# Kernel tuning notes

Measured on AMD Instinct MI355X. Metric: run time of the kernel, lower is better.

The kernel has to match this reference:

```python
import jax, jax.numpy as jnp
import numpy as np

BS = 4
N_NODES = 10000
N_FEAT = 64
HID = 128
N_LAYERS = 4
HID_FC = 512
N_CLASSES = 10
N_EDGES = 160000


def setup_inputs() -> dict:
    key = jax.random.key(0)
    ks = jax.random.split(key, 10)
    x = jax.random.normal(ks[0], (BS, N_NODES, N_FEAT), jnp.float32)
    edge_index = jax.random.randint(ks[1], (2, N_EDGES), 0, N_NODES, dtype=jnp.int32)
    # batch[b*N_NODES + i] = b, matching x.view(num_nodes*bs, -1) row-major flatten
    batch = jnp.repeat(jnp.arange(BS, dtype=jnp.int32), N_NODES)
    W1 = jax.random.normal(ks[2], (N_FEAT, HID), jnp.float32) * (N_FEAT ** -0.5)
    b1 = jax.random.normal(ks[3], (HID,), jnp.float32) * 0.01
    Ws = jax.random.normal(ks[4], (N_LAYERS - 1, HID, HID), jnp.float32) * (HID ** -0.5)
    bconvs = jax.random.normal(ks[5], (N_LAYERS - 1, HID), jnp.float32) * 0.01
    lin1_w = jax.random.normal(ks[6], (N_LAYERS * HID, HID_FC), jnp.float32) * ((N_LAYERS * HID) ** -0.5)
    lin1_b = jax.random.normal(ks[7], (HID_FC,), jnp.float32) * 0.01
    lin2_w = jax.random.normal(ks[8], (HID_FC, N_CLASSES), jnp.float32) * (HID_FC ** -0.5)
    lin2_b = jax.random.normal(ks[9], (N_CLASSES,), jnp.float32) * 0.01
    return {"x": x, "edge_index": edge_index, "batch": batch,
            "W1": W1, "b1": b1, "Ws": Ws, "bconvs": bconvs,
            "lin1_w": lin1_w, "lin1_b": lin1_b, "lin2_w": lin2_w, "lin2_b": lin2_b}


def _gcn_norm(edge_index, n):
    # PyG GCNConv: add self-loops, symmetric normalization D^-1/2 (A+I) D^-1/2
    loops = jnp.arange(n, dtype=edge_index.dtype)
    src = jnp.concatenate([edge_index[0], loops])
    dst = jnp.concatenate([edge_index[1], loops])
    deg = jnp.zeros((n,), jnp.float32).at[dst].add(1.0)
    dinv = jnp.where(deg > 0, jax.lax.rsqrt(deg), 0.0)
    return src, dst, dinv[src] * dinv[dst]


def reference(x, edge_index, batch, W1, b1, Ws, bconvs, lin1_w, lin1_b, lin2_w, lin2_b):
    bs, n, _ = x.shape
    src, dst, norm = _gcn_norm(edge_index, n)

    def gcn(h, W, b):
        m = (h @ W)[:, src, :] * norm[None, :, None]          # [bs, E+n, H]
        agg = jax.vmap(lambda mm: jax.ops.segment_sum(mm, dst, num_segments=n))(m)
        return agg + b

    h = jax.nn.relu(gcn(x, W1, b1))
    xs = [h]
    for i in range(Ws.shape[0]):
        h = jax.nn.relu(gcn(h, Ws[i], bconvs[i]))
        xs.append(h)
    # torch.stack(xs, -1).view(bs, n, -1): per-channel layer interleave
    h = jnp.stack(xs, -1).reshape(bs, n, -1)                   # [bs, n, L*H]
    flat = h.reshape(bs * n, -1)
    summed = jax.ops.segment_sum(flat, batch, num_segments=bs)
    counts = jax.ops.segment_sum(jnp.ones((bs * n,), flat.dtype), batch, num_segments=bs)
    pooled = summed / counts[:, None]                          # global_mean_pool
    h = jax.nn.relu(pooled @ lin1_w + lin1_b)
    # dropout p=0.5 is inference-disabled (training=False)
    logits = h @ lin2_w + lin2_b
    return jax.nn.log_softmax(logits, axis=-1)
```

## Files before the change

### kernel.cpp

```cpp
#include <hip/hip_runtime.h>
#include <hip/hip_bf16.h>
#include <math.h>

#define N_NODES 10000
#define N_EDGES 160000
#define BS      4
#define N_TOT   (BS * N_NODES)
#define HID     128
#define NPC     10
#define CHUNKS  (N_NODES/NPC)
#define HID_FC  512
#define N_CLASSES 10
#define N_LAYERS  4
#define DEG_CAP 64

using bf16x8 = __attribute__((ext_vector_type(8))) short;
using f32x4  = __attribute__((ext_vector_type(4))) float;

__device__ __forceinline__ float bf_lo(unsigned u) { return __uint_as_float(u << 16); }
__device__ __forceinline__ float bf_hi(unsigned u) { return __uint_as_float(u & 0xffff0000u); }
__device__ __forceinline__ unsigned bf_rne(float x) {
    unsigned b = __float_as_uint(x);
    return (b + 0x7fffu + ((b >> 16) & 1u)) >> 16;
}
__device__ __forceinline__ float bf2f(unsigned hi16) { return __uint_as_float(hi16 << 16); }


__global__ void k_init(int4* p, int n4) {
    int i = blockIdx.x * 256 + threadIdx.x;
    if (i < n4) p[i] = make_int4(0, 0, 0, 0);
}

__global__ void k_count(const int* __restrict__ ei, int* __restrict__ counts) {
    int e = blockIdx.x * 256 + threadIdx.x;
    if (e < N_EDGES) atomicAdd(&counts[ei[N_EDGES + e]], 1);
}

__global__ void k_dinv(const int* __restrict__ counts, float* __restrict__ dinv) {
    int i = blockIdx.x * 256 + threadIdx.x;
    if (i < N_NODES) dinv[i] = rsqrtf((float)(counts[i] + 1));
}

__global__ void k_fill(const int* __restrict__ ei, int* __restrict__ cursor,
                       const float* __restrict__ dinv, int2* __restrict__ csr) {
    int e = blockIdx.x * 256 + threadIdx.x;
    if (e < N_EDGES) {
        int s = ei[e], d = ei[N_EDGES + e];
        int pos = atomicAdd(&cursor[d], 1);
        if (pos < DEG_CAP)
            csr[(d << 6) + pos] = make_int2(s, __float_as_int(dinv[s]));
    }
}

#define XB 2500
__global__ void k_cvt(const float* __restrict__ x, const float* __restrict__ W1,
                      const float* __restrict__ Ws, ushort* __restrict__ x_bf,
                      ushort* __restrict__ wt_hi, ushort* __restrict__ wt_lo) {
    int bid = blockIdx.x, t = threadIdx.x;
    if (bid < XB) {
        int i = bid * 256 + t;
        float4 v = ((const float4*)x)[i];
        ushort4 o;
        o.x = (ushort)bf_rne(v.x); o.y = (ushort)bf_rne(v.y);
        o.z = (ushort)bf_rne(v.z); o.w = (ushort)bf_rne(v.w);
        ((ushort4*)x_bf)[i] = o;
    } else {
        int idx = (bid - XB) * 256 + t;
        float v;
        if (idx < 128 * 64) {
            int c = idx >> 6, k = idx & 63;
            v = W1[k * HID + c];
        } else {
            int tt = idx - 128 * 64;
            int li = tt >> 14, rem = tt & 16383;
            int c = rem >> 7, k = rem & 127;
            v = Ws[li * 16384 + k * HID + c];
        }
        unsigned hi = bf_rne(v);
        unsigned lo = bf_rne(v - bf2f(hi));
        wt_hi[idx] = (ushort)hi;
        wt_lo[idx] = (ushort)lo;
    }
}

template<int K>
__global__ __launch_bounds__(256) void k_mm(const ushort* __restrict__ A,
                                            const ushort* __restrict__ Bt_hi,
                                            const ushort* __restrict__ Bt_lo,
                                            ushort* __restrict__ outB) {
    constexpr int NS = K / 32;
    const int lane = threadIdx.x & 63;
    const int w    = threadIdx.x >> 6;
    const int row_base = blockIdx.x * 128 + w * 32;
    const int lr = lane & 15, lg = lane >> 4;

    bf16x8 a[2][NS];
    #pragma unroll
    for (int rh = 0; rh < 2; ++rh) {
        int r = row_base + rh * 16 + lr;
        if (r > N_TOT - 1) r = N_TOT - 1;
        const ushort* ap = A + (size_t)r * K + lg * 8;
        #pragma unroll
        for (int s = 0; s < NS; ++s)
            a[rh][s] = *(const bf16x8*)(ap + s * 32);
    }

    f32x4 acc[2][8];
    #pragma unroll
    for (int rh = 0; rh < 2; ++rh)
        #pragma unroll
        for (int n = 0; n < 8; ++n)
            acc[rh][n] = (f32x4){0.f, 0.f, 0.f, 0.f};

    #pragma unroll
    for (int n = 0; n < 8; ++n) {
        const ushort* bp = Bt_hi + (size_t)(n * 16 + lr) * K + lg * 8;
        const ushort* bq = Bt_lo + (size_t)(n * 16 + lr) * K + lg * 8;
        #pragma unroll
        for (int s = 0; s < NS; ++s) {
            bf16x8 bh = *(const bf16x8*)(bp + s * 32);
            bf16x8 bl = *(const bf16x8*)(bq + s * 32);
            acc[0][n] = __builtin_amdgcn_mfma_f32_16x16x32_bf16(a[0][s], bh, acc[0][n], 0, 0, 0);
            acc[1][n] = __builtin_amdgcn_mfma_f32_16x16x32_bf16(a[1][s], bh, acc[1][n], 0, 0, 0);
            acc[0][n] = __builtin_amdgcn_mfma_f32_16x16x32_bf16(a[0][s], bl, acc[0][n], 0, 0, 0);
            acc[1][n] = __builtin_amdgcn_mfma_f32_16x16x32_bf16(a[1][s], bl, acc[1][n], 0, 0, 0);
        }
    }

    #pragma unroll
    for (int rh = 0; rh < 2; ++rh) {
        int rb = row_base + rh * 16 + lg * 4;
        #pragma unroll
        for (int n = 0; n < 8; ++n) {
            int col = n * 16 + lr;
            #pragma unroll
            for (int j = 0; j < 4; ++j) {
                int r = rb + j;
                if (r < N_TOT)
                    outB[(size_t)r * HID + col] = (ushort)bf_rne(acc[rh][n][j]);
            }
        }
    }
}

__global__ __launch_bounds__(128) void k_aggregate(const unsigned* __restrict__ tmpw,
                                                   const int* __restrict__ counts,
                                                   const int2* __restrict__ csr,
                                                   const float* __restrict__ dinv,
                                                   const float* __restrict__ bias,
                                                   unsigned* __restrict__ houtw,
                                                   float* __restrict__ partial) {
    const int id = blockIdx.x;
    const int b = (id & 7) >> 1;
    const int chunk = ((id >> 3) << 1) | (id & 1);
    const int w = threadIdx.x >> 6, l = threadIdx.x & 63;
    const unsigned* tb = tmpw + (size_t)b * N_NODES * 64;
    const float2 bv = ((const float2*)bias)[l];
    float2 pool = {0.f, 0.f};
    const int n0 = chunk * NPC + w * (NPC / 2);
    for (int n = n0; n < n0 + NPC / 2; ++n) {
        int cnt = counts[n];
        if (cnt > DEG_CAP) cnt = DEG_CAP;
        const int no = (cnt + 7) >> 3;
        const float dn = dinv[n];
        unsigned us = tb[(size_t)n * 64 + l];
        float ax[8], ay[8];
        ax[0] = dn * bf_lo(us); ay[0] = dn * bf_hi(us);
        #pragma unroll
        for (int i = 1; i < 8; ++i) { ax[i] = 0.f; ay[i] = 0.f; }
        const int4* cp = (const int4*)(csr + ((size_t)n << 6));
        for (int q = 0; q < no; ++q) {
            int4 q0 = cp[4 * q], q1 = cp[4 * q + 1], q2 = cp[4 * q + 2], q3 = cp[4 * q + 3];
            unsigned u0 = tb[(size_t)q0.x * 64 + l];
            unsigned u1 = tb[(size_t)q0.z * 64 + l];
            unsigned u2 = tb[(size_t)q1.x * 64 + l];
            unsigned u3 = tb[(size_t)q1.z * 64 + l];
            unsigned u4 = tb[(size_t)q2.x * 64 + l];
            unsigned u5 = tb[(size_t)q2.z * 64 + l];
            unsigned u6 = tb[(size_t)q3.x * 64 + l];
            unsigned u7 = tb[(size_t)q3.z * 64 + l];
            float w0 = __int_as_float(q0.y), w1 = __int_as_float(q0.w);
            float w2 = __int_as_float(q1.y), w3 = __int_as_float(q1.w);
            float w4 = __int_as_float(q2.y), w5 = __int_as_float(q2.w);
            float w6 = __int_as_float(q3.y), w7 = __int_as_float(q3.w);
            ax[0] = fmaf(w0, bf_lo(u0), ax[0]); ay[0] = fmaf(w0, bf_hi(u0), ay[0]);
            ax[1] = fmaf(w1, bf_lo(u1), ax[1]); ay[1] = fmaf(w1, bf_hi(u1), ay[1]);
            ax[2] = fmaf(w2, bf_lo(u2), ax[2]); ay[2] = fmaf(w2, bf_hi(u2), ay[2]);
            ax[3] = fmaf(w3, bf_lo(u3), ax[3]); ay[3] = fmaf(w3, bf_hi(u3), ay[3]);
            ax[4] = fmaf(w4, bf_lo(u4), ax[4]); ay[4] = fmaf(w4, bf_hi(u4), ay[4]);
            ax[5] = fmaf(w5, bf_lo(u5), ax[5]); ay[5] = fmaf(w5, bf_hi(u5), ay[5]);
            ax[6] = fmaf(w6, bf_lo(u6), ax[6]); ay[6] = fmaf(w6, bf_hi(u6), ay[6]);
            ax[7] = fmaf(w7, bf_lo(u7), ax[7]); ay[7] = fmaf(w7, bf_hi(u7), ay[7]);
        }
        float sx = ((ax[0] + ax[1]) + (ax[2] + ax[3])) + ((ax[4] + ax[5]) + (ax[6] + ax[7]));
        float sy = ((ay[0] + ay[1]) + (ay[2] + ay[3])) + ((ay[4] + ay[5]) + (ay[6] + ay[7]));
        float rx = fmaxf(fmaf(dn, sx, bv.x), 0.f);
        float ry = fmaxf(fmaf(dn, sy, bv.y), 0.f);
        houtw[((size_t)b * N_NODES + n) * 64 + l] = bf_rne(rx) | (bf_rne(ry) << 16);
        pool.x += rx; pool.y += ry;
    }
    __shared__ float2 pw[64];
    if (w == 1) pw[l] = pool;
    __syncthreads();
    if (w == 0) {
        pool.x += pw[l].x; pool.y += pw[l].y;
        ((float2*)partial)[((size_t)b * CHUNKS + chunk) * 64 + l] = pool;
    }
}

__global__ void k_reduce(const float* __restrict__ partial, float* __restrict__ pooled) {
    int l = blockIdx.x >> 2, b = blockIdx.x & 3, c = threadIdx.x;
    const float* p = partial + (size_t)(l * BS + b) * CHUNKS * HID + c;
    float s0 = 0, s1 = 0, s2 = 0, s3 = 0;
    for (int ch = 0; ch < CHUNKS; ch += 4) {
        s0 += p[(ch + 0) * HID];
        s1 += p[(ch + 1) * HID];
        s2 += p[(ch + 2) * HID];
        s3 += p[(ch + 3) * HID];
    }
    pooled[(size_t)(l * BS + b) * HID + c] = ((s0 + s1) + (s2 + s3)) * (1.0f / N_NODES);
}

__global__ __launch_bounds__(256) void k_lin1(const float* __restrict__ pooled,
                                              const float* __restrict__ w,
                                              const float* __restrict__ bias,
                                              float* __restrict__ h1) {
    __shared__ float pf[BS][HID_FC];
    __shared__ float red[8][32][BS];
    const int t = threadIdx.x;
    const int o0 = blockIdx.x * 32;
    for (int i = t; i < BS * HID_FC; i += 256) {
        int b = i >> 9, f = i & 511;
        int l = f & 3, cc = f >> 2;
        pf[b][f] = pooled[(size_t)(l * BS + b) * HID + cc];
    }
    __syncthreads();
    const int o = t & 31, kq = t >> 5;
    float acc[BS] = {0.f, 0.f, 0.f, 0.f};
    #pragma unroll 4
    for (int k = kq * 64; k < kq * 64 + 64; ++k) {
        float wv = w[(size_t)k * HID_FC + o0 + o];
        #pragma unroll
        for (int b = 0; b < BS; ++b) acc[b] = fmaf(pf[b][k], wv, acc[b]);
    }
    #pragma unroll
    for (int b = 0; b < BS; ++b) red[kq][o][b] = acc[b];
    __syncthreads();
    if (t < 128) {
        int oo = t & 31, b = t >> 5;
        float s = 0.f;
        #pragma unroll
        for (int q = 0; q < 8; ++q) s += red[q][oo][b];
        s += bias[o0 + oo];
        h1[(size_t)b * HID_FC + o0 + oo] = fmaxf(s, 0.f);
    }
}

__global__ __launch_bounds__(512) void k_lin2(const float* __restrict__ h1,
                                              const float* __restrict__ w,
                                              const float* __restrict__ bias,
                                              float* __restrict__ out) {
    const int k = threadIdx.x;
    const int lane = k & 63, wv_id = k >> 6;
    float wrow[N_CLASSES];
    #pragma unroll
    for (int c = 0; c < N_CLASSES; ++c) wrow[c] = w[k * N_CLASSES + c];
    float hv[BS];
    #pragma unroll
    for (int b = 0; b < BS; ++b) hv[b] = h1[b * HID_FC + k];
    float acc[BS][N_CLASSES];
    #pragma unroll
    for (int b = 0; b < BS; ++b)
        #pragma unroll
        for (int c = 0; c < N_CLASSES; ++c) acc[b][c] = hv[b] * wrow[c];
    #pragma unroll
    for (int off = 32; off >= 1; off >>= 1) {
        #pragma unroll
        for (int b = 0; b < BS; ++b)
            #pragma unroll
            for (int c = 0; c < N_CLASSES; ++c)
                acc[b][c] += __shfl_down(acc[b][c], off);
    }
    __shared__ float red[8][BS * N_CLASSES];
    if (lane == 0) {
        #pragma unroll
        for (int b = 0; b < BS; ++b)
            #pragma unroll
            for (int c = 0; c < N_CLASSES; ++c)
                red[wv_id][b * N_CLASSES + c] = acc[b][c];
    }
    __syncthreads();
    __shared__ float logits[BS][N_CLASSES];
    if (k < BS * N_CLASSES) {
        int b = k / N_CLASSES, c = k % N_CLASSES;
        float s = bias[c];
        #pragma unroll
        for (int q = 0; q < 8; ++q) s += red[q][k];
        logits[b][c] = s;
    }
    __syncthreads();
    if (k < BS) {
        float m = logits[k][0];
        for (int i = 1; i < N_CLASSES; ++i) m = fmaxf(m, logits[k][i]);
        float s = 0.f;
        for (int i = 0; i < N_CLASSES; ++i) s += expf(logits[k][i] - m);
        float lse = m + logf(s);
        for (int i = 0; i < N_CLASSES; ++i) out[k * N_CLASSES + i] = logits[k][i] - lse;
    }
}

extern "C" void kernel_launch(void* const* d_in, const int* in_sizes, int n_in,
                              void* d_out, int out_size, void* d_ws, size_t ws_size,
                              hipStream_t stream) {
    const float* x       = (const float*)d_in[0];
    const int*   ei      = (const int*)d_in[1];
    const float* W1      = (const float*)d_in[3];
    const float* b1      = (const float*)d_in[4];
    const float* Ws      = (const float*)d_in[5];
    const float* bconvs  = (const float*)d_in[6];
    const float* lin1_w  = (const float*)d_in[7];
    const float* lin1_b  = (const float*)d_in[8];
    const float* lin2_w  = (const float*)d_in[9];
    const float* lin2_b  = (const float*)d_in[10];
    float* out = (float*)d_out;

    char* base = (char*)d_ws;
    ushort* tmp16  = (ushort*)base;                      base += (size_t)N_TOT * HID * 2;
    ushort* hA16   = (ushort*)base;                      base += (size_t)N_TOT * HID * 2;
    ushort* x_bf   = (ushort*)base;                      base += (size_t)N_TOT * 64 * 2;
    ushort* wt_hi  = (ushort*)base;                      base += 57344 * 2;
    ushort* wt_lo  = (ushort*)base;                      base += 57344 * 2;
    float*  partial= (float*)base;                       base += (size_t)N_LAYERS * BS * CHUNKS * HID * 4;
    float*  pooled = (float*)base;                       base += N_LAYERS * BS * HID * 4;
    float*  h1     = (float*)base;                       base += BS * HID_FC * 4;
    float*  dinv   = (float*)base;                       base += N_NODES * 4;
    int*    counts = (int*)base;                         base += N_NODES * 4;
    int*    cursor = (int*)base;                         base += N_NODES * 4;
    int2*   csr    = (int2*)base;

    const int GE = (N_EDGES + 255) / 256;
    const int zero_ints = 2 * N_NODES + 2 * N_NODES * DEG_CAP;
    const int n4 = zero_ints / 4;

    k_init<<<(n4 + 255) / 256, 256, 0, stream>>>((int4*)counts, n4);
    k_count<<<GE, 256, 0, stream>>>(ei, counts);
    k_dinv<<<(N_NODES + 255) / 256, 256, 0, stream>>>(counts, dinv);
    k_fill<<<GE, 256, 0, stream>>>(ei, cursor, dinv, csr);
    k_cvt<<<XB + 224, 256, 0, stream>>>(x, W1, Ws, x_bf, wt_hi, wt_lo);

    const int agg_grid = BS * CHUNKS;
    const int mm_grid = (N_TOT + 127) / 128;

    k_mm<64><<<mm_grid, 256, 0, stream>>>(x_bf, wt_hi, wt_lo, tmp16);
    k_aggregate<<<agg_grid, 128, 0, stream>>>((unsigned*)tmp16, counts, csr, dinv, b1,
                                              (unsigned*)hA16, partial);
    for (int l = 1; l < N_LAYERS; ++l) {
        const ushort* whi = wt_hi + 8192 + (size_t)(l - 1) * 16384;
        const ushort* wlo = wt_lo + 8192 + (size_t)(l - 1) * 16384;
        const float* bl = bconvs + (size_t)(l - 1) * HID;
        k_mm<128><<<mm_grid, 256, 0, stream>>>(hA16, whi, wlo, tmp16);
        k_aggregate<<<agg_grid, 128, 0, stream>>>((unsigned*)tmp16, counts, csr, dinv, bl,
                                                  (unsigned*)hA16,
                                                  partial + (size_t)l * BS * CHUNKS * HID);
    }

    k_reduce<<<N_LAYERS * BS, HID, 0, stream>>>(partial, pooled);
    k_lin1<<<HID_FC / 32, 256, 0, stream>>>(pooled, lin1_w, lin1_b, h1);
    k_lin2<<<1, 512, 0, stream>>>(h1, lin2_w, lin2_b, out);
}
```

Measured before the change: 270.3 us.

## Replace fixed-cap CSR with compact padded CSR and interleave two-node aggregation

Builds a compact CSR with per-node rows padded to multiples of 4, allocated by an atomic bump counter, instead of a fixed 64-slot-per-node array. This removes the large zero-init and the degree cap. It fuses the zero-init, x conversion and weight split into one grid-stride prep kernel, drops the separate dinv kernel by computing rsqrt inline, and processes two nodes per iteration in the aggregation for more memory-level parallelism. NPC changes to 8. Rows are allocated by atomics, so their order is nondeterministic and locality between adjacent nodes' edge lists is lost. Padding slots rely on being zeroed (zero weight, source index 0).

```diff
diff --git a/kernel.cpp b/kernel.cpp
--- a/kernel.cpp
+++ b/kernel.cpp
@@ -7,12 +7,13 @@
 #define BS      4
 #define N_TOT   (BS * N_NODES)
 #define HID     128
-#define NPC     10
+#define NPC     8
 #define CHUNKS  (N_NODES/NPC)
 #define HID_FC  512
 #define N_CLASSES 10
 #define N_LAYERS  4
-#define DEG_CAP 64
+#define CSR_CAP 190000
+#define ZERO_INT4 102501
 
 using bf16x8 = __attribute__((ext_vector_type(8))) short;
 using f32x4  = __attribute__((ext_vector_type(4))) float;
@@ -25,61 +26,60 @@
 }
 __device__ __forceinline__ float bf2f(unsigned hi16) { return __uint_as_float(hi16 << 16); }
 
-
-__global__ void k_init(int4* p, int n4) {
-    int i = blockIdx.x * 256 + threadIdx.x;
-    if (i < n4) p[i] = make_int4(0, 0, 0, 0);
-}
-
-__global__ void k_count(const int* __restrict__ ei, int* __restrict__ counts) {
-    int e = blockIdx.x * 256 + threadIdx.x;
-    if (e < N_EDGES) atomicAdd(&counts[ei[N_EDGES + e]], 1);
-}
-
-__global__ void k_dinv(const int* __restrict__ counts, float* __restrict__ dinv) {
-    int i = blockIdx.x * 256 + threadIdx.x;
-    if (i < N_NODES) dinv[i] = rsqrtf((float)(counts[i] + 1));
-}
-
-__global__ void k_fill(const int* __restrict__ ei, int* __restrict__ cursor,
-                       const float* __restrict__ dinv, int2* __restrict__ csr) {
-    int e = blockIdx.x * 256 + threadIdx.x;
-    if (e < N_EDGES) {
-        int s = ei[e], d = ei[N_EDGES + e];
-        int pos = atomicAdd(&cursor[d], 1);
-        if (pos < DEG_CAP)
-            csr[(d << 6) + pos] = make_int2(s, __float_as_int(dinv[s]));
-    }
-}
-
-#define XB 2500
-__global__ void k_cvt(const float* __restrict__ x, const float* __restrict__ W1,
-                      const float* __restrict__ Ws, ushort* __restrict__ x_bf,
-                      ushort* __restrict__ wt_hi, ushort* __restrict__ wt_lo) {
-    int bid = blockIdx.x, t = threadIdx.x;
-    if (bid < XB) {
-        int i = bid * 256 + t;
+__global__ __launch_bounds__(256) void k_prep(const float* __restrict__ x,
+                                              const float* __restrict__ W1,
+                                              const float* __restrict__ Ws,
+                                              int4* __restrict__ zbase,
+                                              ushort* __restrict__ x_bf,
+                                              ushort* __restrict__ wt_hi,
+                                              ushort* __restrict__ wt_lo) {
+    const int gt = blockIdx.x * 256 + threadIdx.x, NT = gridDim.x * 256;
+    for (int i = gt; i < ZERO_INT4; i += NT) zbase[i] = make_int4(0, 0, 0, 0);
+    for (int i = gt; i < 640000; i += NT) {
         float4 v = ((const float4*)x)[i];
         ushort4 o;
         o.x = (ushort)bf_rne(v.x); o.y = (ushort)bf_rne(v.y);
         o.z = (ushort)bf_rne(v.z); o.w = (ushort)bf_rne(v.w);
         ((ushort4*)x_bf)[i] = o;
-    } else {
-        int idx = (bid - XB) * 256 + t;
+    }
+    for (int i = gt; i < 57344; i += NT) {
         float v;
-        if (idx < 128 * 64) {
-            int c = idx >> 6, k = idx & 63;
-            v = W1[k * HID + c];
-        } else {
-            int tt = idx - 128 * 64;
-            int li = tt >> 14, rem = tt & 16383;
+        if (i < 8192) { int c = i >> 6, k = i & 63; v = W1[k * HID + c]; }
+        else {
+            int tt = i - 8192, li = tt >> 14, rem = tt & 16383;
             int c = rem >> 7, k = rem & 127;
             v = Ws[li * 16384 + k * HID + c];
         }
         unsigned hi = bf_rne(v);
         unsigned lo = bf_rne(v - bf2f(hi));
-        wt_hi[idx] = (ushort)hi;
-        wt_lo[idx] = (ushort)lo;
+        wt_hi[i] = (ushort)hi;
+        wt_lo[i] = (ushort)lo;
+    }
+}
+
+__global__ void k_count(const int* __restrict__ ei, int* __restrict__ counts) {
+    int e = blockIdx.x * 256 + threadIdx.x;
+    if (e < N_EDGES) atomicAdd(&counts[ei[N_EDGES + e]], 1);
+}
+
+__global__ void k_alloc(const int* __restrict__ counts, int* __restrict__ row_start,
+                        int* __restrict__ g_total) {
+    int i = blockIdx.x * 256 + threadIdx.x;
+    if (i < N_NODES) {
+        int padded = (counts[i] + 3) & ~3;
+        row_start[i] = atomicAdd(g_total, padded);
+    }
+}
+
+__global__ void k_fill(const int* __restrict__ ei, const int* __restrict__ counts,
+                       const int* __restrict__ row_start, int* __restrict__ cursor,
+                       int2* __restrict__ csr) {
+    int e = blockIdx.x * 256 + threadIdx.x;
+    if (e < N_EDGES) {
+        int s = ei[e], d = ei[N_EDGES + e];
+        float ws = rsqrtf((float)(counts[s] + 1));
+        int pos = atomicAdd(&cursor[d], 1);
+        csr[row_start[d] + pos] = make_int2(s, __float_as_int(ws));
     }
 }
 
@@ -143,13 +143,13 @@
     }
 }
 
-__global__ __launch_bounds__(128) void k_aggregate(const unsigned* __restrict__ tmpw,
-                                                   const int* __restrict__ counts,
-                                                   const int2* __restrict__ csr,
-                                                   const float* __restrict__ dinv,
-                                                   const float* __restrict__ bias,
-                                                   unsigned* __restrict__ houtw,
-                                                   float* __restrict__ partial) {
+__global__ __launch_bounds__(128) void k_agg(const unsigned* __restrict__ tmpw,
+                                             const int* __restrict__ counts,
+                                             const int* __restrict__ row_start,
+                                             const int2* __restrict__ csr,
+                                             const float* __restrict__ bias,
+                                             unsigned* __restrict__ houtw,
+                                             float* __restrict__ partial) {
     const int id = blockIdx.x;
     const int b = (id & 7) >> 1;
     const int chunk = ((id >> 3) << 1) | (id & 1);
@@ -157,48 +157,74 @@
     const unsigned* tb = tmpw + (size_t)b * N_NODES * 64;
     const float2 bv = ((const float2*)bias)[l];
     float2 pool = {0.f, 0.f};
-    const int n0 = chunk * NPC + w * (NPC / 2);
-    for (int n = n0; n < n0 + NPC / 2; ++n) {
-        int cnt = counts[n];
-        if (cnt > DEG_CAP) cnt = DEG_CAP;
-        const int no = (cnt + 7) >> 3;
-        const float dn = dinv[n];
-        unsigned us = tb[(size_t)n * 64 + l];
-        float ax[8], ay[8];
-        ax[0] = dn * bf_lo(us); ay[0] = dn * bf_hi(us);
-        #pragma unroll
-        for (int i = 1; i < 8; ++i) { ax[i] = 0.f; ay[i] = 0.f; }
-        const int4* cp = (const int4*)(csr + ((size_t)n << 6));
-        for (int q = 0; q < no; ++q) {
-            int4 q0 = cp[4 * q], q1 = cp[4 * q + 1], q2 = cp[4 * q + 2], q3 = cp[4 * q + 3];
-            unsigned u0 = tb[(size_t)q0.x * 64 + l];
-            unsigned u1 = tb[(size_t)q0.z * 64 + l];
-            unsigned u2 = tb[(size_t)q1.x * 64 + l];
-            unsigned u3 = tb[(size_t)q1.z * 64 + l];
-            unsigned u4 = tb[(size_t)q2.x * 64 + l];
-            unsigned u5 = tb[(size_t)q2.z * 64 + l];
-            unsigned u6 = tb[(size_t)q3.x * 64 + l];
-            unsigned u7 = tb[(size_t)q3.z * 64 + l];
-            float w0 = __int_as_float(q0.y), w1 = __int_as_float(q0.w);
-            float w2 = __int_as_float(q1.y), w3 = __int_as_float(q1.w);
-            float w4 = __int_as_float(q2.y), w5 = __int_as_float(q2.w);
-            float w6 = __int_as_float(q3.y), w7 = __int_as_float(q3.w);
-            ax[0] = fmaf(w0, bf_lo(u0), ax[0]); ay[0] = fmaf(w0, bf_hi(u0), ay[0]);
-            ax[1] = fmaf(w1, bf_lo(u1), ax[1]); ay[1] = fmaf(w1, bf_hi(u1), ay[1]);
-            ax[2] = fmaf(w2, bf_lo(u2), ax[2]); ay[2] = fmaf(w2, bf_hi(u2), ay[2]);
-            ax[3] = fmaf(w3, bf_lo(u3), ax[3]); ay[3] = fmaf(w3, bf_hi(u3), ay[3]);
-            ax[4] = fmaf(w4, bf_lo(u4), ax[4]); ay[4] = fmaf(w4, bf_hi(u4), ay[4]);
-            ax[5] = fmaf(w5, bf_lo(u5), ax[5]); ay[5] = fmaf(w5, bf_hi(u5), ay[5]);
-            ax[6] = fmaf(w6, bf_lo(u6), ax[6]); ay[6] = fmaf(w6, bf_hi(u6), ay[6]);
-            ax[7] = fmaf(w7, bf_lo(u7), ax[7]); ay[7] = fmaf(w7, bf_hi(u7), ay[7]);
-        }
-        float sx = ((ax[0] + ax[1]) + (ax[2] + ax[3])) + ((ax[4] + ax[5]) + (ax[6] + ax[7]));
-        float sy = ((ay[0] + ay[1]) + (ay[2] + ay[3])) + ((ay[4] + ay[5]) + (ay[6] + ay[7]));
-        float rx = fmaxf(fmaf(dn, sx, bv.x), 0.f);
-        float ry = fmaxf(fmaf(dn, sy, bv.y), 0.f);
-        houtw[((size_t)b * N_NODES + n) * 64 + l] = bf_rne(rx) | (bf_rne(ry) << 16);
-        pool.x += rx; pool.y += ry;
-    }
+    const int n0 = chunk * NPC + w * 4;
+
+    #pragma unroll
+    for (int pn = 0; pn < 2; ++pn) {
+        const int nA = n0 + 2 * pn, nB = nA + 1;
+        const int cntA = counts[nA], cntB = counts[nB];
+        const int baseA = row_start[nA], baseB = row_start[nB];
+        const float dnA = rsqrtf((float)(cntA + 1));
+        const float dnB = rsqrtf((float)(cntB + 1));
+        const unsigned usA = tb[(size_t)nA * 64 + l];
+        const unsigned usB = tb[(size_t)nB * 64 + l];
+        float axA[4], ayA[4], axB[4], ayB[4];
+        axA[0] = dnA * bf_lo(usA); ayA[0] = dnA * bf_hi(usA);
+        axB[0] = dnB * bf_lo(usB); ayB[0] = dnB * bf_hi(usB);
+        #pragma unroll
+        for (int i = 1; i < 4; ++i) { axA[i] = 0.f; ayA[i] = 0.f; axB[i] = 0.f; ayB[i] = 0.f; }
+        const int nqA = (cntA + 3) >> 2, nqB = (cntB + 3) >> 2;
+        const int nq = nqA > nqB ? nqA : nqB;
+        const int4* cpA = (const int4*)(csr + baseA);
+        const int4* cpB = (const int4*)(csr + baseB);
+        for (int q = 0; q < nq; ++q) {
+            const bool doA = q < nqA, doB = q < nqB;
+            int4 qa0, qa1, qb0, qb1;
+            if (doA) { qa0 = cpA[2 * q]; qa1 = cpA[2 * q + 1]; }
+            if (doB) { qb0 = cpB[2 * q]; qb1 = cpB[2 * q + 1]; }
+            if (doA) {
+                unsigned u0 = tb[(size_t)qa0.x * 64 + l];
+                unsigned u1 = tb[(size_t)qa0.z * 64 + l];
+                unsigned u2 = tb[(size_t)qa1.x * 64 + l];
+                unsigned u3 = tb[(size_t)qa1.z * 64 + l];
+                float w0 = __int_as_float(qa0.y), w1 = __int_as_float(qa0.w);
+                float w2 = __int_as_float(qa1.y), w3 = __int_as_float(qa1.w);
+                axA[0] = fmaf(w0, bf_lo(u0), axA[0]); ayA[0] = fmaf(w0, bf_hi(u0), ayA[0]);
+                axA[1] = fmaf(w1, bf_lo(u1), axA[1]); ayA[1] = fmaf(w1, bf_hi(u1), ayA[1]);
+                axA[2] = fmaf(w2, bf_lo(u2), axA[2]); ayA[2] = fmaf(w2, bf_hi(u2), ayA[2]);
+                axA[3] = fmaf(w3, bf_lo(u3), axA[3]); ayA[3] = fmaf(w3, bf_hi(u3), ayA[3]);
+            }
+            if (doB) {
+                unsigned u0 = tb[(size_t)qb0.x * 64 + l];
+                unsigned u1 = tb[(size_t)qb0.z * 64 + l];
+                unsigned u2 = tb[(size_t)qb1.x * 64 + l];
+                unsigned u3 = tb[(size_t)qb1.z * 64 + l];
+                float w0 = __int_as_float(qb0.y), w1 = __int_as_float(qb0.w);
+                float w2 = __int_as_float(qb1.y), w3 = __int_as_float(qb1.w);
+                axB[0] = fmaf(w0, bf_lo(u0), axB[0]); ayB[0] = fmaf(w0, bf_hi(u0), ayB[0]);
+                axB[1] = fmaf(w1, bf_lo(u1), axB[1]); ayB[1] = fmaf(w1, bf_hi(u1), ayB[1]);
+                axB[2] = fmaf(w2, bf_lo(u2), axB[2]); ayB[2] = fmaf(w2, bf_hi(u2), ayB[2]);
+                axB[3] = fmaf(w3, bf_lo(u3), axB[3]); ayB[3] = fmaf(w3, bf_hi(u3), ayB[3]);
+            }
+        }
+        {
+            float sx = (axA[0] + axA[1]) + (axA[2] + axA[3]);
+            float sy = (ayA[0] + ayA[1]) + (ayA[2] + ayA[3]);
+            float rx = fmaxf(fmaf(dnA, sx, bv.x), 0.f);
+            float ry = fmaxf(fmaf(dnA, sy, bv.y), 0.f);
+            houtw[((size_t)b * N_NODES + nA) * 64 + l] = bf_rne(rx) | (bf_rne(ry) << 16);
+            pool.x += rx; pool.y += ry;
+        }
+        {
+            float sx = (axB[0] + axB[1]) + (axB[2] + axB[3]);
+            float sy = (ayB[0] + ayB[1]) + (ayB[2] + ayB[3]);
+            float rx = fmaxf(fmaf(dnB, sx, bv.x), 0.f);
+            float ry = fmaxf(fmaf(dnB, sy, bv.y), 0.f);
+            houtw[((size_t)b * N_NODES + nB) * 64 + l] = bf_rne(rx) | (bf_rne(ry) << 16);
+            pool.x += rx; pool.y += ry;
+        }
+    }
+
     __shared__ float2 pw[64];
     if (w == 1) pw[l] = pool;
     __syncthreads();
@@ -211,14 +237,12 @@
 __global__ void k_reduce(const float* __restrict__ partial, float* __restrict__ pooled) {
     int l = blockIdx.x >> 2, b = blockIdx.x & 3, c = threadIdx.x;
     const float* p = partial + (size_t)(l * BS + b) * CHUNKS * HID + c;
-    float s0 = 0, s1 = 0, s2 = 0, s3 = 0;
-    for (int ch = 0; ch < CHUNKS; ch += 4) {
+    float s0 = 0, s1 = 0;
+    for (int ch = 0; ch < CHUNKS; ch += 2) {
         s0 += p[(ch + 0) * HID];
         s1 += p[(ch + 1) * HID];
-        s2 += p[(ch + 2) * HID];
-        s3 += p[(ch + 3) * HID];
-    }
-    pooled[(size_t)(l * BS + b) * HID + c] = ((s0 + s1) + (s2 + s3)) * (1.0f / N_NODES);
+    }
+    pooled[(size_t)(l * BS + b) * HID + c] = (s0 + s1) * (1.0f / N_NODES);
 }
 
 __global__ __launch_bounds__(256) void k_lin1(const float* __restrict__ pooled,
@@ -325,43 +349,41 @@
     float* out = (float*)d_out;
 
     char* base = (char*)d_ws;
-    ushort* tmp16  = (ushort*)base;                      base += (size_t)N_TOT * HID * 2;
-    ushort* hA16   = (ushort*)base;                      base += (size_t)N_TOT * HID * 2;
-    ushort* x_bf   = (ushort*)base;                      base += (size_t)N_TOT * 64 * 2;
-    ushort* wt_hi  = (ushort*)base;                      base += 57344 * 2;
-    ushort* wt_lo  = (ushort*)base;                      base += 57344 * 2;
-    float*  partial= (float*)base;                       base += (size_t)N_LAYERS * BS * CHUNKS * HID * 4;
-    float*  pooled = (float*)base;                       base += N_LAYERS * BS * HID * 4;
-    float*  h1     = (float*)base;                       base += BS * HID_FC * 4;
-    float*  dinv   = (float*)base;                       base += N_NODES * 4;
-    int*    counts = (int*)base;                         base += N_NODES * 4;
-    int*    cursor = (int*)base;                         base += N_NODES * 4;
-    int2*   csr    = (int2*)base;
+    ushort* tmp16   = (ushort*)base;   base += (size_t)N_TOT * HID * 2;
+    ushort* hA16    = (ushort*)base;   base += (size_t)N_TOT * HID * 2;
+    ushort* x_bf    = (ushort*)base;   base += (size_t)N_TOT * 64 * 2;
+    ushort* wt_hi   = (ushort*)base;   base += 57344 * 2;
+    ushort* wt_lo   = (ushort*)base;   base += 57344 * 2;
+    float*  partial = (float*)base;    base += (size_t)N_LAYERS * BS * CHUNKS * HID * 4;
+    float*  pooled  = (float*)base;    base += N_LAYERS * BS * HID * 4;
+    float*  h1      = (float*)base;    base += BS * HID_FC * 4;
+    int*    counts    = (int*)base;    base += N_NODES * 4;
+    int*    cursor    = (int*)base;    base += N_NODES * 4;
+    int*    row_start = (int*)base;    base += N_NODES * 4;
+    int*    g_total   = (int*)base;    base += 4 * 4;
+    int2*   csr       = (int2*)base;
 
     const int GE = (N_EDGES + 255) / 256;
-    const int zero_ints = 2 * N_NODES + 2 * N_NODES * DEG_CAP;
-    const int n4 = zero_ints / 4;
-
-    k_init<<<(n4 + 255) / 256, 256, 0, stream>>>((int4*)counts, n4);
+
+    k_prep<<<1024, 256, 0, stream>>>(x, W1, Ws, (int4*)counts, x_bf, wt_hi, wt_lo);
     k_count<<<GE, 256, 0, stream>>>(ei, counts);
-    k_dinv<<<(N_NODES + 255) / 256, 256, 0, stream>>>(counts, dinv);
-    k_fill<<<GE, 256, 0, stream>>>(ei, cursor, dinv, csr);
-    k_cvt<<<XB + 224, 256, 0, stream>>>(x, W1, Ws, x_bf, wt_hi, wt_lo);
+    k_alloc<<<(N_NODES + 255) / 256, 256, 0, stream>>>(counts, row_start, g_total);
+    k_fill<<<GE, 256, 0, stream>>>(ei, counts, row_start, cursor, csr);
 
     const int agg_grid = BS * CHUNKS;
     const int mm_grid = (N_TOT + 127) / 128;
 
     k_mm<64><<<mm_grid, 256, 0, stream>>>(x_bf, wt_hi, wt_lo, tmp16);
-    k_aggregate<<<agg_grid, 128, 0, stream>>>((unsigned*)tmp16, counts, csr, dinv, b1,
-                                              (unsigned*)hA16, partial);
+    k_agg<<<agg_grid, 128, 0, stream>>>((unsigned*)tmp16, counts, row_start, csr, b1,
+                                        (unsigned*)hA16, partial);
     for (int l = 1; l < N_LAYERS; ++l) {
         const ushort* whi = wt_hi + 8192 + (size_t)(l - 1) * 16384;
         const ushort* wlo = wt_lo + 8192 + (size_t)(l - 1) * 16384;
         const float* bl = bconvs + (size_t)(l - 1) * HID;
         k_mm<128><<<mm_grid, 256, 0, stream>>>(hA16, whi, wlo, tmp16);
-        k_aggregate<<<agg_grid, 128, 0, stream>>>((unsigned*)tmp16, counts, csr, dinv, bl,
-                                                  (unsigned*)hA16,
-                                                  partial + (size_t)l * BS * CHUNKS * HID);
+        k_agg<<<agg_grid, 128, 0, stream>>>((unsigned*)tmp16, counts, row_start, csr, bl,
+                                            (unsigned*)hA16,
+                                            partial + (size_t)l * BS * CHUNKS * HID);
     }
 
     k_reduce<<<N_LAYERS * BS, HID, 0, stream>>>(partial, pooled);
```

New measurement: 309.6 us. +14.6%, slower.

## Store transformed features as FP8 and merge preprocessing kernels

Applied to the files above, without the earlier changes.

The per-layer h@W intermediate is now stored as FP8 e4m3 instead of bf16, which halves the bytes gathered per edge in the aggregation kernel. It is decoded with hardware cvt_pk builtins when they are available and a software fallback otherwise. The init, dinv and convert kernels are folded into one grid-stride prep kernel, and dinv is recomputed inline from the counts. This cuts launch count and memory traffic at the cost of noticeably lower intermediate precision, which may hurt accuracy tolerance.

```diff
diff --git a/kernel.cpp b/kernel.cpp
--- a/kernel.cpp
+++ b/kernel.cpp
@@ -13,73 +13,108 @@
 #define N_CLASSES 10
 #define N_LAYERS  4
 #define DEG_CAP 64
+#define ZERO_INT4 325000
 
 using bf16x8 = __attribute__((ext_vector_type(8))) short;
 using f32x4  = __attribute__((ext_vector_type(4))) float;
-
-__device__ __forceinline__ float bf_lo(unsigned u) { return __uint_as_float(u << 16); }
-__device__ __forceinline__ float bf_hi(unsigned u) { return __uint_as_float(u & 0xffff0000u); }
+using f32x2  = __attribute__((ext_vector_type(2))) float;
+
 __device__ __forceinline__ unsigned bf_rne(float x) {
     unsigned b = __float_as_uint(x);
     return (b + 0x7fffu + ((b >> 16) & 1u)) >> 16;
 }
 __device__ __forceinline__ float bf2f(unsigned hi16) { return __uint_as_float(hi16 << 16); }
 
-
-__global__ void k_init(int4* p, int n4) {
-    int i = blockIdx.x * 256 + threadIdx.x;
-    if (i < n4) p[i] = make_int4(0, 0, 0, 0);
-}
-
-__global__ void k_count(const int* __restrict__ ei, int* __restrict__ counts) {
-    int e = blockIdx.x * 256 + threadIdx.x;
-    if (e < N_EDGES) atomicAdd(&counts[ei[N_EDGES + e]], 1);
-}
-
-__global__ void k_dinv(const int* __restrict__ counts, float* __restrict__ dinv) {
-    int i = blockIdx.x * 256 + threadIdx.x;
-    if (i < N_NODES) dinv[i] = rsqrtf((float)(counts[i] + 1));
-}
-
-__global__ void k_fill(const int* __restrict__ ei, int* __restrict__ cursor,
-                       const float* __restrict__ dinv, int2* __restrict__ csr) {
-    int e = blockIdx.x * 256 + threadIdx.x;
-    if (e < N_EDGES) {
-        int s = ei[e], d = ei[N_EDGES + e];
-        int pos = atomicAdd(&cursor[d], 1);
-        if (pos < DEG_CAP)
-            csr[(d << 6) + pos] = make_int2(s, __float_as_int(dinv[s]));
-    }
-}
-
-#define XB 2500
-__global__ void k_cvt(const float* __restrict__ x, const float* __restrict__ W1,
-                      const float* __restrict__ Ws, ushort* __restrict__ x_bf,
-                      ushort* __restrict__ wt_hi, ushort* __restrict__ wt_lo) {
-    int bid = blockIdx.x, t = threadIdx.x;
-    if (bid < XB) {
-        int i = bid * 256 + t;
+#if __has_builtin(__builtin_amdgcn_cvt_pk_f32_fp8) && __has_builtin(__builtin_amdgcn_cvt_pk_fp8_f32)
+#define HW_FP8 1
+#else
+#define HW_FP8 0
+#endif
+
+__device__ __forceinline__ float fp8_dec1(unsigned b) {
+    unsigned s = (b & 0x80u) << 24;
+    unsigned em = b & 0x7Fu;
+    float mag;
+    if (em >= 8u) mag = __uint_as_float((((em >> 3) + 120u) << 23) | ((em & 7u) << 20));
+    else          mag = (float)em * 0x1p-9f;
+    return __uint_as_float(s | __float_as_uint(mag));
+}
+
+__device__ __forceinline__ unsigned fp8_enc(float x) {
+#if HW_FP8
+    return (unsigned)(__builtin_amdgcn_cvt_pk_fp8_f32(x, x, 0, false) & 0xFF);
+#else
+    unsigned s = (__float_as_uint(x) >> 24) & 0x80u;
+    float ax = fabsf(x);
+    unsigned r;
+    if (ax >= 0x1p-6f) {
+        if (ax > 448.f) r = 0x7Eu;
+        else {
+            unsigned b = __float_as_uint(ax);
+            unsigned t = b + 0x7FFFFu + ((b >> 20) & 1u);
+            r = (t >> 20) - 960u;
+        }
+    } else {
+        r = (unsigned)__float2int_rn(ax * 512.f);
+    }
+    return s | r;
+#endif
+}
+
+__device__ __forceinline__ float2 fp8x2_dec(unsigned u) {
+#if HW_FP8
+    f32x2 r = __builtin_amdgcn_cvt_pk_f32_fp8((int)(u & 0xFFFFu), false);
+    return make_float2(r[0], r[1]);
+#else
+    return make_float2(fp8_dec1(u & 0xFFu), fp8_dec1((u >> 8) & 0xFFu));
+#endif
+}
+
+__global__ __launch_bounds__(256) void k_prep(const float* __restrict__ x,
+                                              const float* __restrict__ W1,
+                                              const float* __restrict__ Ws,
+                                              int4* __restrict__ zbase,
+                                              ushort* __restrict__ x_bf,
+                                              ushort* __restrict__ wt_hi,
+                                              ushort* __restrict__ wt_lo) {
+    const int gt = blockIdx.x * 256 + threadIdx.x, NT = gridDim.x * 256;
+    for (int i = gt; i < ZERO_INT4; i += NT) zbase[i] = make_int4(0, 0, 0, 0);
+    for (int i = gt; i < 640000; i += NT) {
         float4 v = ((const float4*)x)[i];
         ushort4 o;
         o.x = (ushort)bf_rne(v.x); o.y = (ushort)bf_rne(v.y);
         o.z = (ushort)bf_rne(v.z); o.w = (ushort)bf_rne(v.w);
         ((ushort4*)x_bf)[i] = o;
-    } else {
-        int idx = (bid - XB) * 256 + t;
+    }
+    for (int i = gt; i < 57344; i += NT) {
         float v;
-        if (idx < 128 * 64) {
-            int c = idx >> 6, k = idx & 63;
-            v = W1[k * HID + c];
-        } else {
-            int tt = idx - 128 * 64;
-            int li = tt >> 14, rem = tt & 16383;
+        if (i < 8192) { int c = i >> 6, k = i & 63; v = W1[k * HID + c]; }
+        else {
+            int tt = i - 8192, li = tt >> 14, rem = tt & 16383;
             int c = rem >> 7, k = rem & 127;
             v = Ws[li * 16384 + k * HID + c];
         }
         unsigned hi = bf_rne(v);
         unsigned lo = bf_rne(v - bf2f(hi));
-        wt_hi[idx] = (ushort)hi;
-        wt_lo[idx] = (ushort)lo;
+        wt_hi[i] = (ushort)hi;
+        wt_lo[i] = (ushort)lo;
+    }
+}
+
+__global__ void k_count(const int* __restrict__ ei, int* __restrict__ counts) {
+    int e = blockIdx.x * 256 + threadIdx.x;
+    if (e < N_EDGES) atomicAdd(&counts[ei[N_EDGES + e]], 1);
+}
+
+__global__ void k_fill(const int* __restrict__ ei, const int* __restrict__ counts,
+                       int* __restrict__ cursor, int2* __restrict__ csr) {
+    int e = blockIdx.x * 256 + threadIdx.x;
+    if (e < N_EDGES) {
+        int s = ei[e], d = ei[N_EDGES + e];
+        float ws = rsqrtf((float)(counts[s] + 1));
+        int pos = atomicAdd(&cursor[d], 1);
+        if (pos < DEG_CAP)
+            csr[(d << 6) + pos] = make_int2(s, __float_as_int(ws));
     }
 }
 
@@ -87,7 +122,7 @@
 __global__ __launch_bounds__(256) void k_mm(const ushort* __restrict__ A,
                                             const ushort* __restrict__ Bt_hi,
                                             const ushort* __restrict__ Bt_lo,
-                                            ushort* __restrict__ outB) {
+                                            unsigned char* __restrict__ outF8) {
     constexpr int NS = K / 32;
     const int lane = threadIdx.x & 63;
     const int w    = threadIdx.x >> 6;
@@ -137,35 +172,34 @@
             for (int j = 0; j < 4; ++j) {
                 int r = rb + j;
                 if (r < N_TOT)
-                    outB[(size_t)r * HID + col] = (ushort)bf_rne(acc[rh][n][j]);
+                    outF8[(size_t)r * HID + col] = (unsigned char)fp8_enc(acc[rh][n][j]);
             }
         }
     }
 }
 
-__global__ __launch_bounds__(128) void k_aggregate(const unsigned* __restrict__ tmpw,
-                                                   const int* __restrict__ counts,
-                                                   const int2* __restrict__ csr,
-                                                   const float* __restrict__ dinv,
-                                                   const float* __restrict__ bias,
-                                                   unsigned* __restrict__ houtw,
-                                                   float* __restrict__ partial) {
+__global__ __launch_bounds__(128) void k_agg(const ushort* __restrict__ tmp8,
+                                             const int* __restrict__ counts,
+                                             const int2* __restrict__ csr,
+                                             const float* __restrict__ bias,
+                                             unsigned* __restrict__ houtw,
+                                             float* __restrict__ partial) {
     const int id = blockIdx.x;
     const int b = (id & 7) >> 1;
     const int chunk = ((id >> 3) << 1) | (id & 1);
     const int w = threadIdx.x >> 6, l = threadIdx.x & 63;
-    const unsigned* tb = tmpw + (size_t)b * N_NODES * 64;
+    const ushort* tb = tmp8 + (size_t)b * N_NODES * 64;
     const float2 bv = ((const float2*)bias)[l];
     float2 pool = {0.f, 0.f};
     const int n0 = chunk * NPC + w * (NPC / 2);
     for (int n = n0; n < n0 + NPC / 2; ++n) {
         int cnt = counts[n];
+        const float dn = rsqrtf((float)(cnt + 1));
         if (cnt > DEG_CAP) cnt = DEG_CAP;
         const int no = (cnt + 7) >> 3;
-        const float dn = dinv[n];
-        unsigned us = tb[(size_t)n * 64 + l];
+        const float2 self = fp8x2_dec(tb[(size_t)n * 64 + l]);
         float ax[8], ay[8];
-        ax[0] = dn * bf_lo(us); ay[0] = dn * bf_hi(us);
+        ax[0] = dn * self.x; ay[0] = dn * self.y;
         #pragma unroll
         for (int i = 1; i < 8; ++i) { ax[i] = 0.f; ay[i] = 0.f; }
         const int4* cp = (const int4*)(csr + ((size_t)n << 6));
@@ -183,14 +217,18 @@
             float w2 = __int_as_float(q1.y), w3 = __int_as_float(q1.w);
             float w4 = __int_as_float(q2.y), w5 = __int_as_float(q2.w);
             float w6 = __int_as_float(q3.y), w7 = __int_as_float(q3.w);
-            ax[0] = fmaf(w0, bf_lo(u0), ax[0]); ay[0] = fmaf(w0, bf_hi(u0), ay[0]);
-            ax[1] = fmaf(w1, bf_lo(u1), ax[1]); ay[1] = fmaf(w1, bf_hi(u1), ay[1]);
-            ax[2] = fmaf(w2, bf_lo(u2), ax[2]); ay[2] = fmaf(w2, bf_hi(u2), ay[2]);
-            ax[3] = fmaf(w3, bf_lo(u3), ax[3]); ay[3] = fmaf(w3, bf_hi(u3), ay[3]);
-            ax[4] = fmaf(w4, bf_lo(u4), ax[4]); ay[4] = fmaf(w4, bf_hi(u4), ay[4]);
-            ax[5] = fmaf(w5, bf_lo(u5), ax[5]); ay[5] = fmaf(w5, bf_hi(u5), ay[5]);
-            ax[6] = fmaf(w6, bf_lo(u6), ax[6]); ay[6] = fmaf(w6, bf_hi(u6), ay[6]);
-            ax[7] = fmaf(w7, bf_lo(u7), ax[7]); ay[7] = fmaf(w7, bf_hi(u7), ay[7]);
+            float2 f0 = fp8x2_dec(u0), f1 = fp8x2_dec(u1);
+            float2 f2 = fp8x2_dec(u2), f3 = fp8x2_dec(u3);
+            float2 f4 = fp8x2_dec(u4), f5 = fp8x2_dec(u5);
+            float2 f6 = fp8x2_dec(u6), f7 = fp8x2_dec(u7);
+            ax[0] = fmaf(w0, f0.x, ax[0]); ay[0] = fmaf(w0, f0.y, ay[0]);
+            ax[1] = fmaf(w1, f1.x, ax[1]); ay[1] = fmaf(w1, f1.y, ay[1]);
+            ax[2] = fmaf(w2, f2.x, ax[2]); ay[2] = fmaf(w2, f2.y, ay[2]);
+            ax[3] = fmaf(w3, f3.x, ax[3]); ay[3] = fmaf(w3, f3.y, ay[3]);
+            ax[4] = fmaf(w4, f4.x, ax[4]); ay[4] = fmaf(w4, f4.y, ay[4]);
+            ax[5] = fmaf(w5, f5.x, ax[5]); ay[5] = fmaf(w5, f5.y, ay[5]);
+            ax[6] = fmaf(w6, f6.x, ax[6]); ay[6] = fmaf(w6, f6.y, ay[6]);
+            ax[7] = fmaf(w7, f7.x, ax[7]); ay[7] = fmaf(w7, f7.y, ay[7]);
         }
         float sx = ((ax[0] + ax[1]) + (ax[2] + ax[3])) + ((ax[4] + ax[5]) + (ax[6] + ax[7]));
         float sy = ((ay[0] + ay[1]) + (ay[2] + ay[3])) + ((ay[4] + ay[5]) + (ay[6] + ay[7]));
@@ -325,43 +363,38 @@
     float* out = (float*)d_out;
 
     char* base = (char*)d_ws;
-    ushort* tmp16  = (ushort*)base;                      base += (size_t)N_TOT * HID * 2;
-    ushort* hA16   = (ushort*)base;                      base += (size_t)N_TOT * HID * 2;
-    ushort* x_bf   = (ushort*)base;                      base += (size_t)N_TOT * 64 * 2;
-    ushort* wt_hi  = (ushort*)base;                      base += 57344 * 2;
-    ushort* wt_lo  = (ushort*)base;                      base += 57344 * 2;
-    float*  partial= (float*)base;                       base += (size_t)N_LAYERS * BS * CHUNKS * HID * 4;
-    float*  pooled = (float*)base;                       base += N_LAYERS * BS * HID * 4;
-    float*  h1     = (float*)base;                       base += BS * HID_FC * 4;
-    float*  dinv   = (float*)base;                       base += N_NODES * 4;
-    int*    counts = (int*)base;                         base += N_NODES * 4;
-    int*    cursor = (int*)base;                         base += N_NODES * 4;
+    unsigned char* tmp8 = (unsigned char*)base; base += (size_t)N_TOT * HID;
+    ushort* hA16   = (ushort*)base;    base += (size_t)N_TOT * HID * 2;
+    ushort* x_bf   = (ushort*)base;    base += (size_t)N_TOT * 64 * 2;
+    ushort* wt_hi  = (ushort*)base;    base += 57344 * 2;
+    ushort* wt_lo  = (ushort*)base;    base += 57344 * 2;
+    float*  partial= (float*)base;     base += (size_t)N_LAYERS * BS * CHUNKS * HID * 4;
+    float*  pooled = (float*)base;     base += N_LAYERS * BS * HID * 4;
+    float*  h1     = (float*)base;     base += BS * HID_FC * 4;
+    int*    counts = (int*)base;       base += N_NODES * 4;
+    int*    cursor = (int*)base;       base += N_NODES * 4;
     int2*   csr    = (int2*)base;
 
     const int GE = (N_EDGES + 255) / 256;
-    const int zero_ints = 2 * N_NODES + 2 * N_NODES * DEG_CAP;
-    const int n4 = zero_ints / 4;
-
-    k_init<<<(n4 + 255) / 256, 256, 0, stream>>>((int4*)counts, n4);
+
+    k_prep<<<1024, 256, 0, stream>>>(x, W1, Ws, (int4*)counts, x_bf, wt_hi, wt_lo);
     k_count<<<GE, 256, 0, stream>>>(ei, counts);
-    k_dinv<<<(N_NODES + 255) / 256, 256, 0, stream>>>(counts, dinv);
-    k_fill<<<GE, 256, 0, stream>>>(ei, cursor, dinv, csr);
-    k_cvt<<<XB + 224, 256, 0, stream>>>(x, W1, Ws, x_bf, wt_hi, wt_lo);
+    k_fill<<<GE, 256, 0, stream>>>(ei, counts, cursor, csr);
 
     const int agg_grid = BS * CHUNKS;
     const int mm_grid = (N_TOT + 127) / 128;
 
-    k_mm<64><<<mm_grid, 256, 0, stream>>>(x_bf, wt_hi, wt_lo, tmp16);
-    k_aggregate<<<agg_grid, 128, 0, stream>>>((unsigned*)tmp16, counts, csr, dinv, b1,
-                                              (unsigned*)hA16, partial);
+    k_mm<64><<<mm_grid, 256, 0, stream>>>(x_bf, wt_hi, wt_lo, tmp8);
+    k_agg<<<agg_grid, 128, 0, stream>>>((const ushort*)tmp8, counts, csr, b1,
+                                        (unsigned*)hA16, partial);
     for (int l = 1; l < N_LAYERS; ++l) {
         const ushort* whi = wt_hi + 8192 + (size_t)(l - 1) * 16384;
         const ushort* wlo = wt_lo + 8192 + (size_t)(l - 1) * 16384;
         const float* bl = bconvs + (size_t)(l - 1) * HID;
-        k_mm<128><<<mm_grid, 256, 0, stream>>>(hA16, whi, wlo, tmp16);
-        k_aggregate<<<agg_grid, 128, 0, stream>>>((unsigned*)tmp16, counts, csr, dinv, bl,
-                                                  (unsigned*)hA16,
-                                                  partial + (size_t)l * BS * CHUNKS * HID);
+        k_mm<128><<<mm_grid, 256, 0, stream>>>(hA16, whi, wlo, tmp8);
+        k_agg<<<agg_grid, 128, 0, stream>>>((const ushort*)tmp8, counts, csr, bl,
+                                            (unsigned*)hA16,
+                                            partial + (size_t)l * BS * CHUNKS * HID);
     }
 
     k_reduce<<<N_LAYERS * BS, HID, 0, stream>>>(partial, pooled);
```

New measurement: 254.5 us. 5.9% less time.
